# Kernel tuning notes

Hardware: AMD Instinct MI355X
Metric: run time of the kernel (lower is better)

Reference implementation:

```python
import jax, jax.numpy as jnp
import numpy as np

B, L, D = 2048, 96, 256  # groups, max group size, feature dim
COUNTS = np.tile(np.array([32, 64, 96, 64], dtype=np.int64), B // 4)  # ragged sizes, max=96
E = int(COUNTS.sum())  # 131072 edges


def setup_inputs() -> dict:
    key = jax.random.key(0)
    ks = jax.random.split(key, 12)
    s = 1.0 / np.sqrt(D)
    inp = {
        "x": jax.random.normal(ks[0], (E, D), jnp.float32),
        "timestamps_": jax.random.uniform(ks[1], (E,), jnp.float32),
    }
    names = ["w_ih_l0", "w_hh_l0", "b_ih_l0", "b_hh_l0",
             "w_ih_l1", "w_hh_l1", "b_ih_l1", "b_hh_l1"]
    shapes = [(3 * D, D), (3 * D, D), (3 * D,), (3 * D,),
              (3 * D, D), (3 * D, D), (3 * D,), (3 * D,)]
    for i, (n, sh) in enumerate(zip(names, shapes)):
        inp[n] = jax.random.uniform(ks[2 + i], sh, jnp.float32, -s, s)
    inp["index"] = jnp.asarray(np.repeat(np.arange(B), COUNTS), dtype=jnp.int32)
    return inp


def _gru_layer(seq, w_ih, w_hh, b_ih, b_hh):
    # seq: [B, L, F]; PyTorch gate order: r, z, n
    H = w_hh.shape[1]
    xp = jnp.einsum('blf,gf->blg', seq, w_ih) + b_ih  # precompute input GEMM, [B, L, 3H]

    def step(h, x_t):
        gh = h @ w_hh.T + b_hh  # [B, 3H]
        xr, xz, xn = jnp.split(x_t, 3, axis=-1)
        hr, hz, hn = jnp.split(gh, 3, axis=-1)
        r = jax.nn.sigmoid(xr + hr)
        z = jax.nn.sigmoid(xz + hz)
        n = jnp.tanh(xn + r * hn)
        h_new = (1 - z) * n + z * h
        return h_new, h_new

    h0 = jnp.zeros((seq.shape[0], H), seq.dtype)
    _, ys = jax.lax.scan(step, h0, jnp.swapaxes(xp, 0, 1))  # scan over time
    return jnp.swapaxes(ys, 0, 1)  # [B, L, H]


def reference(x, timestamps_, w_ih_l0, w_hh_l0, b_ih_l0, b_hh_l0,
              w_ih_l1, w_hh_l1, b_ih_l1, b_hh_l1, index):
    # prepend timestamp column: [E, D+1]
    feats = jnp.concatenate([timestamps_[:, None], x], axis=1)
    # to_dense_batch: sort by group, scatter into [B, L, D+1] (zero-padded)
    sort_ids = jnp.argsort(index)
    si = index[sort_ids]
    counts = jax.ops.segment_sum(jnp.ones((E,), jnp.int32), index, num_segments=B)
    offsets = jnp.cumsum(counts) - counts  # exclusive cumsum
    pos = jnp.arange(E, dtype=jnp.int32) - offsets[si]  # position within group
    dense = jnp.zeros((B, L, D + 1), feats.dtype).at[si, pos].set(feats[sort_ids])
    # sort each group by timestamp (column 0; padded zeros sort first), drop timestamp
    order = jnp.argsort(dense[:, :, 0], axis=1)
    seq = jnp.take_along_axis(dense, order[:, :, None], axis=1)[:, :, 1:]  # [B, L, D]
    # 2-layer GRU + mean pool over time
    h1 = _gru_layer(seq, w_ih_l0, w_hh_l0, b_ih_l0, b_hh_l0)
    h2 = _gru_layer(h1, w_ih_l1, w_hh_l1, b_ih_l1, b_hh_l1)
    return h2.mean(axis=1)  # [B, D] (squeeze is a no-op)
```

## Files before the change

kernel.cpp:

```cpp
#include <hip/hip_runtime.h>


typedef short bh8 __attribute__((ext_vector_type(8)));
typedef float f4  __attribute__((ext_vector_type(4)));

#define NB 2048
#define LT 96
#define DF 256
#define NG 768

#define LHA(col, row) (((((col) >> 5) * 64 + (((col) >> 3) & 3) * 16 + (row)) * 8) + ((col) & 7))

static __device__ __forceinline__ unsigned short f2b(float f) {
  union { float f; unsigned int u; } v; v.f = f;
  unsigned int r = v.u + 0x7fffu + ((v.u >> 16) & 1u);
  return (unsigned short)(r >> 16);
}
static __device__ __forceinline__ float b2f(unsigned short s) {
  union { unsigned int u; float f; } v; v.u = ((unsigned int)s) << 16; return v.f;
}
static __device__ __forceinline__ unsigned int pk2(float a, float b) {
  return (unsigned int)f2b(a) | ((unsigned int)f2b(b) << 16);
}
static __device__ __forceinline__ float sigm(float x) { return 1.0f / (1.0f + __expf(-x)); }
static __device__ __forceinline__ float tanh_(float x) { return 2.0f / (1.0f + __expf(-2.0f * x)) - 1.0f; }

__global__ void k_offsets(const int* __restrict__ idx, int E,
                          int* __restrict__ offs, int* __restrict__ cnt) {
  int b = blockIdx.x * blockDim.x + threadIdx.x;
  if (b >= NB) return;
  int lo = 0, hi = E;
  while (lo < hi) { int m = (lo + hi) >> 1; if (idx[m] < b) lo = m + 1; else hi = m; }
  int lb = lo;
  lo = lb; hi = E;
  while (lo < hi) { int m = (lo + hi) >> 1; if (idx[m] < b + 1) lo = m + 1; else hi = m; }
  offs[b] = lb;
  cnt[b] = lo - lb;
}

__global__ void k_rank(const float* __restrict__ ts, const int* __restrict__ offs,
                       const int* __restrict__ cnt, int* __restrict__ perm) {
  __shared__ float sts[96];
  int b = blockIdx.x, j = threadIdx.x;
  int o = offs[b];
  int c = cnt[b]; if (c > 96) c = 96;
  if (j < 96) perm[b * 96 + j] = -1;
  if (j < c) sts[j] = ts[o + j];
  __syncthreads();
  if (j < c) {
    float tj = sts[j];
    int rank = 0;
    for (int k = 0; k < c; ++k) {
      float tk = sts[k];
      rank += (tk < tj) || (tk == tj && k < j);
    }
    int slot = (tj > 0.0f ? (96 - c) : 0) + rank;
    perm[b * 96 + slot] = o + j;
  }
}

__global__ void k_packw(const float* __restrict__ w0, const float* __restrict__ w1,
                        const float* __restrict__ w2, const float* __restrict__ w3,
                        unsigned short* __restrict__ wfrag) {
  int t = blockIdx.x * blockDim.x + threadIdx.x;
  if (t >= 4 * 48 * 8 * 64) return;
  int m = t / 24576;
  int r = t % 24576;
  int nt = r / 512;
  int kt = (r / 64) & 7;
  int lane = r & 63;
  int n = nt * 16 + (lane & 15);
  int kb = kt * 32 + (lane >> 4) * 8;
  const float* W = (m == 0) ? w0 : (m == 1) ? w1 : (m == 2) ? w2 : w3;
  unsigned int o[4];
#pragma unroll
  for (int p = 0; p < 4; ++p)
    o[p] = pk2(W[n * 256 + kb + 2 * p], W[n * 256 + kb + 2 * p + 1]);
  uint4 v; v.x = o[0]; v.y = o[1]; v.z = o[2]; v.w = o[3];
  *(uint4*)&wfrag[(size_t)t * 8] = v;
}

template <int AMODE>
__launch_bounds__(256, 2)
__global__ void k_xgemm(const float* __restrict__ Ax, const unsigned short* __restrict__ Ab,
                        const int* __restrict__ perm, int t0, int slabsTotal, int jbN,
                        const unsigned short* __restrict__ wfrag, const float* __restrict__ bias,
                        unsigned short* __restrict__ Cout) {
  __shared__ float lsm[2][8960];

  const int tid = threadIdx.x;
  const int ntb = blockIdx.x % 6;
  const int jb  = blockIdx.x / 6;
  if (jb >= slabsTotal) return;
  const int w = tid >> 6, l = tid & 63, lm = l & 15, lq = l >> 4;

  const unsigned short* wfN = wfrag + (size_t)ntb * 32768;
  bh8 bf[2][8];
#pragma unroll
  for (int i = 0; i < 2; ++i)
#pragma unroll
    for (int kt = 0; kt < 8; ++kt)
      bf[i][kt] = *(const bh8*)&wfN[(((2 * w + i) * 8 + kt) * 64 + l) * 8];
  const float bias0 = bias[ntb * 128 + (2 * w + 0) * 16 + lm];
  const float bias1 = bias[ntb * 128 + (2 * w + 1) * 16 + lm];

  const int trow = tid >> 2, tp = tid & 3;
  const int msub = trow >> 4, rlm = trow & 15;

  f4 pf[16];
  uint4 pb[8];

  auto issue_loads = [&](int s) {
    int row = s * 64 + trow;
    if (AMODE == 0) {
      int tt = row >> 11, g = row & 2047;
      int src = perm[g * 96 + t0 + tt];
      if (src >= 0) {
        const float* p = Ax + (size_t)src * 256 + tp * 64;
#pragma unroll
        for (int i = 0; i < 16; ++i) pf[i] = *(const f4*)(p + 4 * i);
      } else {
#pragma unroll
        for (int i = 0; i < 16; ++i) pf[i] = (f4){0.f, 0.f, 0.f, 0.f};
      }
    } else {
      const unsigned short* p = Ab + (size_t)row * 256 + tp * 64;
#pragma unroll
      for (int i = 0; i < 8; ++i) pb[i] = *(const uint4*)(p + 8 * i);
    }
  };
  auto write_afrag = [&](int buf) {
    unsigned short* aN = (unsigned short*)lsm[buf];
#pragma unroll
    for (int kk = 0; kk < 2; ++kk)
#pragma unroll
      for (int rlq = 0; rlq < 4; ++rlq) {
        int kt = 2 * tp + kk;
        unsigned short* d = &aN[(((msub * 8 + kt) * 65) + rlq * 16 + rlm) * 8];
        if (AMODE == 0) {
          f4 f0 = pf[8 * kk + 2 * rlq], f1 = pf[8 * kk + 2 * rlq + 1];
          uint4 v;
          v.x = pk2(f0.x, f0.y); v.y = pk2(f0.z, f0.w);
          v.z = pk2(f1.x, f1.y); v.w = pk2(f1.z, f1.w);
          *(uint4*)d = v;
        } else {
          *(uint4*)d = pb[4 * kk + rlq];
        }
      }
  };

  issue_loads(jb);
  write_afrag(0);
  __syncthreads();

  int cur = 0;
  for (int s = jb; s < slabsTotal; s += jbN) {
    const int snext = s + jbN;
    const bool hasNext = snext < slabsTotal;
    if (hasNext) issue_loads(snext);

    const unsigned short* aC = (const unsigned short*)lsm[cur];
    f4 acc[4][2];
#pragma unroll
    for (int m = 0; m < 4; ++m)
#pragma unroll
      for (int n = 0; n < 2; ++n) acc[m][n] = (f4){0.f, 0.f, 0.f, 0.f};
#pragma unroll
    for (int kt = 0; kt < 8; ++kt) {
      bh8 a[4];
#pragma unroll
      for (int m = 0; m < 4; ++m) a[m] = *(const bh8*)&aC[(((m * 8 + kt) * 65) + l) * 8];
#pragma unroll
      for (int m = 0; m < 4; ++m) {
        acc[m][0] = __builtin_amdgcn_mfma_f32_16x16x32_bf16(a[m], bf[0][kt], acc[m][0], 0, 0, 0);
        acc[m][1] = __builtin_amdgcn_mfma_f32_16x16x32_bf16(a[m], bf[1][kt], acc[m][1], 0, 0, 0);
      }
    }

    float* sl = lsm[cur ^ 1];
#pragma unroll
    for (int m = 0; m < 4; ++m)
#pragma unroll
      for (int n = 0; n < 2; ++n) {
        int phys = 36 * w + 16 * n + lm;
        float bv = n ? bias1 : bias0;
#pragma unroll
        for (int r = 0; r < 4; ++r)
          sl[(m * 16 + lq * 4 + r) * 140 + phys] = acc[m][n][r] + bv;
      }
    __syncthreads();

    {
      const float* sp = &sl[trow * 140 + 36 * tp];
      unsigned short* cp = &Cout[((size_t)s * 64 + trow) * NG + ntb * 128 + tp * 32];
#pragma unroll
      for (int i = 0; i < 4; ++i) {
        f4 v0 = *(const f4*)(sp + 8 * i), v1 = *(const f4*)(sp + 8 * i + 4);
        uint4 o;
        o.x = pk2(v0.x, v0.y); o.y = pk2(v0.z, v0.w);
        o.z = pk2(v1.x, v1.y); o.w = pk2(v1.z, v1.w);
        *(uint4*)(cp + 8 * i) = o;
      }
    }
    __syncthreads();

    if (hasNext) {
      write_afrag(cur ^ 1);
      __syncthreads();
    }
    cur ^= 1;
  }
}

template <int LAYER>
__launch_bounds__(512, 2)
__global__ void k_recur(const unsigned short* __restrict__ wf, const float* __restrict__ bhh,
                        const unsigned short* __restrict__ xg, int Ta,
                        float* __restrict__ hstate, int first, int save,
                        unsigned short* __restrict__ h1out,
                        float* __restrict__ sumstate, float* __restrict__ outp, int last) {
  __shared__ __align__(16) unsigned short lBn[32768];
  __shared__ __align__(16) unsigned short lh[2][4096];
  __shared__ __align__(16) unsigned short lxg[2][6144];

  const int tid = threadIdx.x;
  const int w = tid >> 6, l = tid & 63, lm = l & 15, lq = l >> 4;
  const int g0 = blockIdx.x * 8;
  const int colA = w * 32 + lm;
  const int mycol = (lq < 2) ? colA : (colA + 16);
  const int rlow = (lq & 1) * 4;

  bh8 br0[8], br1[8], bz0[8], bz1[8], bn0[8];
#pragma unroll
  for (int kt = 0; kt < 8; ++kt) {
    br0[kt] = *(const bh8*)&wf[(((2 * w + 0) * 8 + kt) * 64 + l) * 8];
    br1[kt] = *(const bh8*)&wf[(((2 * w + 1) * 8 + kt) * 64 + l) * 8];
    bz0[kt] = *(const bh8*)&wf[(((16 + 2 * w) * 8 + kt) * 64 + l) * 8];
    bz1[kt] = *(const bh8*)&wf[(((17 + 2 * w) * 8 + kt) * 64 + l) * 8];
    bn0[kt] = *(const bh8*)&wf[(((32 + 2 * w) * 8 + kt) * 64 + l) * 8];
  }
  const float bhr = bhh[mycol];
  const float bhz = bhh[256 + mycol];
  const float bhn = bhh[512 + mycol];

  {
    for (int i = tid; i < 4096; i += 512) {
      int wp = i >> 9, kt = (i >> 6) & 7, lane = i & 63;
      ((uint4*)lBn)[i] = *(const uint4*)&wf[(((33 + 2 * wp) * 8 + kt) * 64 + lane) * 8];
    }
  }
  {
    uint4 z; z.x = 0u; z.y = 0u; z.z = 0u; z.w = 0u;
    for (int i = tid; i < 1024; i += 512) ((uint4*)lh)[i] = z;
  }
  __syncthreads();

  float hp[4], sm[4];
#pragma unroll
  for (int reg = 0; reg < 4; ++reg) {
    int row = rlow + reg;
    float a = first ? 0.f : hstate[(size_t)(g0 + row) * DF + mycol];
    hp[reg] = a;
    lh[0][LHA(mycol, row)] = f2b(a);
    lh[0][LHA(mycol, row + 8)] = f2b(a);
    if (LAYER == 1) {
      sm[reg] = (!first) ? sumstate[(size_t)(g0 + row) * DF + mycol] : 0.f;
    }
  }
  {
    const unsigned short* gp = xg + (size_t)g0 * NG;
    uint4 q0 = *(const uint4*)(gp + tid * 8);
    *(uint4*)&lxg[0][tid * 8] = q0;
    if (tid < 256) {
      uint4 q1 = *(const uint4*)(gp + 4096 + tid * 8);
      *(uint4*)&lxg[0][4096 + tid * 8] = q1;
    }
  }
  __syncthreads();

  int cur = 0;
  for (int tt = 0; tt < Ta; ++tt) {
    const int nxt = cur ^ 1;
    uint4 p0, p1;
    const bool hasN = (tt + 1 < Ta);
    if (hasN) {
      const unsigned short* gp = xg + ((size_t)(tt + 1) * NB + g0) * NG;
      p0 = *(const uint4*)(gp + tid * 8);
      if (tid < 256) p1 = *(const uint4*)(gp + 4096 + tid * 8);
    }
    if (LAYER == 0 && tt > 0 && tid < 256) {
      int row = tid >> 5, c0 = (tid & 31) * 8;
      uint4 hv = *(const uint4*)&lh[cur][(((c0 >> 5) * 64 + ((c0 >> 3) & 3) * 16 + row) * 8)];
      *(uint4*)&h1out[((size_t)(tt - 1) * NB + g0 + row) * DF + c0] = hv;
    }
    f4 ar0 = (f4){0.f,0.f,0.f,0.f}, ar1 = (f4){0.f,0.f,0.f,0.f};
    f4 az0 = (f4){0.f,0.f,0.f,0.f}, az1 = (f4){0.f,0.f,0.f,0.f};
    f4 an0 = (f4){0.f,0.f,0.f,0.f}, an1 = (f4){0.f,0.f,0.f,0.f};
    const unsigned short* hc = lh[cur];
#pragma unroll
    for (int kt = 0; kt < 8; ++kt) {
      bh8 a = *(const bh8*)&hc[(kt * 64 + l) * 8];
      ar0 = __builtin_amdgcn_mfma_f32_16x16x32_bf16(a, br0[kt], ar0, 0, 0, 0);
      ar1 = __builtin_amdgcn_mfma_f32_16x16x32_bf16(a, br1[kt], ar1, 0, 0, 0);
      az0 = __builtin_amdgcn_mfma_f32_16x16x32_bf16(a, bz0[kt], az0, 0, 0, 0);
      az1 = __builtin_amdgcn_mfma_f32_16x16x32_bf16(a, bz1[kt], az1, 0, 0, 0);
      an0 = __builtin_amdgcn_mfma_f32_16x16x32_bf16(a, bn0[kt], an0, 0, 0, 0);
      bh8 n1 = *(const bh8*)&lBn[((w * 8 + kt) * 64 + l) * 8];
      an1 = __builtin_amdgcn_mfma_f32_16x16x32_bf16(a, n1, an1, 0, 0, 0);
    }
    {
      f4 aR = (lq < 2) ? ar0 : ar1;
      f4 aZ = (lq < 2) ? az0 : az1;
      f4 aN = (lq < 2) ? an0 : an1;
      const unsigned short* xc = lxg[cur];
      unsigned short* hn = lh[nxt];
#pragma unroll
      for (int reg = 0; reg < 4; ++reg) {
        int row = rlow + reg;
        int base = row * NG + mycol;
        float xr = b2f(xc[base]);
        float xz = b2f(xc[base + 256]);
        float xn = b2f(xc[base + 512]);
        float r = sigm(xr + aR[reg] + bhr);
        float z = sigm(xz + aZ[reg] + bhz);
        float n = tanh_(xn + r * (aN[reg] + bhn));
        float h = (1.f - z) * n + z * hp[reg]; hp[reg] = h;
        unsigned short hb = f2b(h);
        hn[LHA(mycol, row)] = hb;
        hn[LHA(mycol, row + 8)] = hb;
        if (LAYER == 1) sm[reg] += h;
      }
    }
    if (hasN) {
      *(uint4*)&lxg[nxt][tid * 8] = p0;
      if (tid < 256) *(uint4*)&lxg[nxt][4096 + tid * 8] = p1;
    }
    __syncthreads();
    cur = nxt;
  }

  if (LAYER == 0 && tid < 256) {
    int row = tid >> 5, c0 = (tid & 31) * 8;
    uint4 hv = *(const uint4*)&lh[cur][(((c0 >> 5) * 64 + ((c0 >> 3) & 3) * 16 + row) * 8)];
    *(uint4*)&h1out[((size_t)(Ta - 1) * NB + g0 + row) * DF + c0] = hv;
  }
  if (save) {
#pragma unroll
    for (int reg = 0; reg < 4; ++reg) {
      int row = rlow + reg;
      hstate[(size_t)(g0 + row) * DF + mycol] = hp[reg];
    }
  }
  if (LAYER == 1) {
    if (last) {
#pragma unroll
      for (int reg = 0; reg < 4; ++reg) {
        int row = rlow + reg;
        outp[(size_t)(g0 + row) * DF + mycol] = sm[reg] * (1.0f / 96.0f);
      }
    } else {
#pragma unroll
      for (int reg = 0; reg < 4; ++reg) {
        int row = rlow + reg;
        sumstate[(size_t)(g0 + row) * DF + mycol] = sm[reg];
      }
    }
  }
}

extern "C" void kernel_launch(void* const* d_in, const int* in_sizes, int n_in,
                              void* d_out, int out_size, void* d_ws, size_t ws_size,
                              hipStream_t stream) {
  (void)n_in; (void)out_size;
  const float* x    = (const float*)d_in[0];
  const float* ts   = (const float*)d_in[1];
  const float* wih0 = (const float*)d_in[2];
  const float* whh0 = (const float*)d_in[3];
  const float* bih0 = (const float*)d_in[4];
  const float* bhh0 = (const float*)d_in[5];
  const float* wih1 = (const float*)d_in[6];
  const float* whh1 = (const float*)d_in[7];
  const float* bih1 = (const float*)d_in[8];
  const float* bhh1 = (const float*)d_in[9];
  const int*   idx  = (const int*)d_in[10];
  float* out = (float*)d_out;
  const int E = in_sizes[0] / DF;

  char* wsb = (char*)d_ws;
  size_t off = 0;
  auto carve = [&](size_t bytes) -> char* {
    off = (off + 255) & ~(size_t)255;
    char* p = wsb + off;
    off += bytes;
    return p;
  };
  int* offs = (int*)carve((size_t)NB * 4);
  int* cntp = (int*)carve((size_t)NB * 4);
  int* perm = (int*)carve((size_t)NB * LT * 4);
  unsigned short* wfrag = (unsigned short*)carve((size_t)4 * 196608 * 2);
  float* h0s  = (float*)carve((size_t)NB * DF * 4);
  float* h1s  = (float*)carve((size_t)NB * DF * 4);
  float* sums = (float*)carve((size_t)NB * DF * 4);
  size_t fixedBytes = off;

  const size_t perT = (size_t)NB * DF * 2 + 2 * (size_t)NB * NG * 2;
  int Tc = 1;
  if (ws_size > fixedBytes + 4096) {
    size_t t = (ws_size - fixedBytes - 4096) / perT;
    Tc = (int)(t > 96 ? 96 : (t < 1 ? 1 : t));
  }
  unsigned short* h1buf = (unsigned short*)carve((size_t)Tc * NB * DF * 2);
  unsigned short* xgA   = (unsigned short*)carve((size_t)Tc * NB * NG * 2);
  unsigned short* xgB   = (unsigned short*)carve((size_t)Tc * NB * NG * 2);

  k_offsets<<<8, 256, 0, stream>>>(idx, E, offs, cntp);
  k_rank<<<NB, 128, 0, stream>>>(ts, offs, cntp, perm);
  k_packw<<<384, 256, 0, stream>>>(wih0, whh0, wih1, whh1, wfrag);

  for (int t0 = 0; t0 < LT; t0 += Tc) {
    int Ta = (LT - t0 < Tc) ? (LT - t0) : Tc;
    int first = (t0 == 0);
    int save = (t0 + Ta < LT);
    int last = (t0 + Ta == LT);
    int slabs = Ta * 32;
    int jbN = slabs < 85 ? slabs : 85;
    k_xgemm<0><<<dim3(6 * jbN), 256, 0, stream>>>(
        x, (const unsigned short*)nullptr, perm, t0, slabs, jbN, wfrag, bih0, xgA);
    k_recur<0><<<256, 512, 0, stream>>>(
        wfrag + 1 * 196608, bhh0, xgA, Ta, h0s, first, save, h1buf,
        (float*)nullptr, (float*)nullptr, 0);
    k_xgemm<1><<<dim3(6 * jbN), 256, 0, stream>>>(
        (const float*)nullptr, h1buf, (const int*)nullptr, 0, slabs, jbN,
        wfrag + 2 * 196608, bih1, xgB);
    k_recur<1><<<256, 512, 0, stream>>>(
        wfrag + 3 * 196608, bhh1, xgB, Ta, h1s, first, save,
        (unsigned short*)nullptr, sums, out, last);
  }
}
```

Before: 1.099 ms.

## Prefetch recurrent input gates three steps ahead via direct global-to-LDS loads

The recurrent kernel now keeps the precomputed input-gate slices in a 4-deep LDS ring filled with global_load_lds, issued three timesteps ahead. Each step waits with hand-tuned per-wave vmcnt counts instead of staging through registers, which takes the global-load latency off the serial recurrence. The input-projection GEMM also walks its slabs in reverse order, probably so the first recurrent steps find their data still in cache. The hand-counted waits are fragile: they depend on how many outstanding vector memory ops each wave has, including the h1out stores in layer 0.

Measured after the change: 1.105 ms. About the same (+0.5%).

```diff
diff --git a/kernel.cpp b/kernel.cpp
--- a/kernel.cpp
+++ b/kernel.cpp
@@ -10,6 +10,27 @@
 #define NG 768
 
 #define LHA(col, row) (((((col) >> 5) * 64 + (((col) >> 3) & 3) * 16 + (row)) * 8) + ((col) & 7))
+
+#define LGKM0()  asm volatile("s_waitcnt lgkmcnt(0)" ::: "memory")
+#define SBAR()   __builtin_amdgcn_s_barrier()
+
+template <int N>
+static __device__ __forceinline__ void vmw() {
+  if constexpr (N == 0)      asm volatile("s_waitcnt vmcnt(0)" ::: "memory");
+  else if constexpr (N == 1) asm volatile("s_waitcnt vmcnt(1)" ::: "memory");
+  else if constexpr (N == 2) asm volatile("s_waitcnt vmcnt(2)" ::: "memory");
+  else if constexpr (N == 3) asm volatile("s_waitcnt vmcnt(3)" ::: "memory");
+  else if constexpr (N == 4) asm volatile("s_waitcnt vmcnt(4)" ::: "memory");
+  else if constexpr (N == 5) asm volatile("s_waitcnt vmcnt(5)" ::: "memory");
+  else if constexpr (N == 6) asm volatile("s_waitcnt vmcnt(6)" ::: "memory");
+  else                       asm volatile("s_waitcnt vmcnt(7)" ::: "memory");
+}
+
+static __device__ __forceinline__ void gl2lds16(const void* g, void* l) {
+  __builtin_amdgcn_global_load_lds(
+      (const __attribute__((address_space(1))) unsigned int*)g,
+      (__attribute__((address_space(3))) unsigned int*)l, 16, 0, 0);
+}
 
 static __device__ __forceinline__ unsigned short f2b(float f) {
   union { float f; unsigned int u; } v; v.f = f;
@@ -111,7 +132,7 @@
   uint4 pb[8];
 
   auto issue_loads = [&](int s) {
-    int row = s * 64 + trow;
+    int row = (slabsTotal - 1 - s) * 64 + trow;
     if (AMODE == 0) {
       int tt = row >> 11, g = row & 2047;
       int src = perm[g * 96 + t0 + tt];
@@ -192,7 +213,7 @@
 
     {
       const float* sp = &sl[trow * 140 + 36 * tp];
-      unsigned short* cp = &Cout[((size_t)s * 64 + trow) * NG + ntb * 128 + tp * 32];
+      unsigned short* cp = &Cout[((size_t)(slabsTotal - 1 - s) * 64 + trow) * NG + ntb * 128 + tp * 32];
 #pragma unroll
       for (int i = 0; i < 4; ++i) {
         f4 v0 = *(const f4*)(sp + 8 * i), v1 = *(const f4*)(sp + 8 * i + 4);
@@ -211,6 +232,64 @@
     cur ^= 1;
   }
 }
+
+#define RSTEP(TT, WLO, WHI, ISSUE, H1, WAIT)                                               \
+  {                                                                                        \
+    if (LAYER == 0 && (H1) && tid < 256) {                                                 \
+      int rw_ = tid >> 5, c0_ = (tid & 31) * 8;                                            \
+      uint4 hv_ = *(const uint4*)&lh[(TT) & 1][(((c0_ >> 5) * 64 + ((c0_ >> 3) & 3) * 16 + rw_) * 8)]; \
+      *(uint4*)&h1out[((size_t)((TT) - 1) * NB + g0 + rw_) * DF + c0_] = hv_;              \
+    }                                                                                      \
+    if (ISSUE) {                                                                           \
+      const unsigned short* gp_ = xg + ((size_t)((TT) + 3) * NB + g0) * NG;                \
+      unsigned short* lb_ = lxg[((TT) + 3) & 3];                                           \
+      gl2lds16(gp_ + (size_t)tid * 8, lb_ + 512 * w);                                      \
+      if (tid < 256) gl2lds16(gp_ + 4096 + (size_t)tid * 8, lb_ + 4096 + 512 * w);         \
+    }                                                                                      \
+    f4 ar0 = (f4){0.f,0.f,0.f,0.f}, ar1 = (f4){0.f,0.f,0.f,0.f};                           \
+    f4 az0 = (f4){0.f,0.f,0.f,0.f}, az1 = (f4){0.f,0.f,0.f,0.f};                           \
+    f4 an0 = (f4){0.f,0.f,0.f,0.f}, an1 = (f4){0.f,0.f,0.f,0.f};                           \
+    {                                                                                      \
+      const unsigned short* hc_ = lh[(TT) & 1];                                            \
+      _Pragma("unroll")                                                                    \
+      for (int kt = 0; kt < 8; ++kt) {                                                     \
+        bh8 a_ = *(const bh8*)&hc_[(kt * 64 + l) * 8];                                     \
+        ar0 = __builtin_amdgcn_mfma_f32_16x16x32_bf16(a_, br0[kt], ar0, 0, 0, 0);          \
+        ar1 = __builtin_amdgcn_mfma_f32_16x16x32_bf16(a_, br1[kt], ar1, 0, 0, 0);          \
+        az0 = __builtin_amdgcn_mfma_f32_16x16x32_bf16(a_, bz0[kt], az0, 0, 0, 0);          \
+        az1 = __builtin_amdgcn_mfma_f32_16x16x32_bf16(a_, bz1[kt], az1, 0, 0, 0);          \
+        an0 = __builtin_amdgcn_mfma_f32_16x16x32_bf16(a_, bn0[kt], an0, 0, 0, 0);          \
+        bh8 n1_ = *(const bh8*)&lBn[((w * 8 + kt) * 64 + l) * 8];                          \
+        an1 = __builtin_amdgcn_mfma_f32_16x16x32_bf16(a_, n1_, an1, 0, 0, 0);              \
+      }                                                                                    \
+    }                                                                                      \
+    {                                                                                      \
+      f4 aR = (lq < 2) ? ar0 : ar1;                                                        \
+      f4 aZ = (lq < 2) ? az0 : az1;                                                        \
+      f4 aN = (lq < 2) ? an0 : an1;                                                        \
+      const unsigned short* xc_ = lxg[(TT) & 3];                                           \
+      unsigned short* hn_ = lh[((TT) & 1) ^ 1];                                            \
+      _Pragma("unroll")                                                                    \
+      for (int reg = 0; reg < 4; ++reg) {                                                  \
+        int row_ = rlow + reg;                                                             \
+        int base_ = row_ * NG + mycol;                                                     \
+        float xr_ = b2f(xc_[base_]);                                                       \
+        float xz_ = b2f(xc_[base_ + 256]);                                                 \
+        float xn_ = b2f(xc_[base_ + 512]);                                                 \
+        float r_ = sigm(xr_ + aR[reg] + bhr);                                              \
+        float z_ = sigm(xz_ + aZ[reg] + bhz);                                              \
+        float n_ = tanh_(xn_ + r_ * (aN[reg] + bhn));                                      \
+        float h_ = (1.f - z_) * n_ + z_ * hp[reg]; hp[reg] = h_;                           \
+        unsigned short hb_ = f2b(h_);                                                      \
+        hn_[LHA(mycol, row_)] = hb_;                                                       \
+        hn_[LHA(mycol, row_ + 8)] = hb_;                                                   \
+        if (LAYER == 1) sm[reg] += h_;                                                     \
+      }                                                                                    \
+    }                                                                                      \
+    LGKM0();                                                                               \
+    if (WAIT) { if (w < 4) { vmw<(WLO)>(); } else { vmw<(WHI)>(); } }                      \
+    SBAR();                                                                                \
+  }
 
 template <int LAYER>
 __launch_bounds__(512, 2)
@@ -221,7 +300,7 @@
                         float* __restrict__ sumstate, float* __restrict__ outp, int last) {
   __shared__ __align__(16) unsigned short lBn[32768];
   __shared__ __align__(16) unsigned short lh[2][4096];
-  __shared__ __align__(16) unsigned short lxg[2][6144];
+  __shared__ __align__(16) unsigned short lxg[4][6144];
 
   const int tid = threadIdx.x;
   const int w = tid >> 6, l = tid & 63, lm = l & 15, lq = l >> 4;
@@ -263,85 +342,50 @@
     hp[reg] = a;
     lh[0][LHA(mycol, row)] = f2b(a);
     lh[0][LHA(mycol, row + 8)] = f2b(a);
-    if (LAYER == 1) {
-      sm[reg] = (!first) ? sumstate[(size_t)(g0 + row) * DF + mycol] : 0.f;
-    }
-  }
-  {
-    const unsigned short* gp = xg + (size_t)g0 * NG;
-    uint4 q0 = *(const uint4*)(gp + tid * 8);
-    *(uint4*)&lxg[0][tid * 8] = q0;
-    if (tid < 256) {
-      uint4 q1 = *(const uint4*)(gp + 4096 + tid * 8);
-      *(uint4*)&lxg[0][4096 + tid * 8] = q1;
-    }
+    if (LAYER == 1) sm[reg] = (!first) ? sumstate[(size_t)(g0 + row) * DF + mycol] : 0.f;
   }
   __syncthreads();
 
-  int cur = 0;
-  for (int tt = 0; tt < Ta; ++tt) {
-    const int nxt = cur ^ 1;
-    uint4 p0, p1;
-    const bool hasN = (tt + 1 < Ta);
-    if (hasN) {
-      const unsigned short* gp = xg + ((size_t)(tt + 1) * NB + g0) * NG;
-      p0 = *(const uint4*)(gp + tid * 8);
-      if (tid < 256) p1 = *(const uint4*)(gp + 4096 + tid * 8);
-    }
-    if (LAYER == 0 && tt > 0 && tid < 256) {
-      int row = tid >> 5, c0 = (tid & 31) * 8;
-      uint4 hv = *(const uint4*)&lh[cur][(((c0 >> 5) * 64 + ((c0 >> 3) & 3) * 16 + row) * 8)];
-      *(uint4*)&h1out[((size_t)(tt - 1) * NB + g0 + row) * DF + c0] = hv;
-    }
-    f4 ar0 = (f4){0.f,0.f,0.f,0.f}, ar1 = (f4){0.f,0.f,0.f,0.f};
-    f4 az0 = (f4){0.f,0.f,0.f,0.f}, az1 = (f4){0.f,0.f,0.f,0.f};
-    f4 an0 = (f4){0.f,0.f,0.f,0.f}, an1 = (f4){0.f,0.f,0.f,0.f};
-    const unsigned short* hc = lh[cur];
-#pragma unroll
-    for (int kt = 0; kt < 8; ++kt) {
-      bh8 a = *(const bh8*)&hc[(kt * 64 + l) * 8];
-      ar0 = __builtin_amdgcn_mfma_f32_16x16x32_bf16(a, br0[kt], ar0, 0, 0, 0);
-      ar1 = __builtin_amdgcn_mfma_f32_16x16x32_bf16(a, br1[kt], ar1, 0, 0, 0);
-      az0 = __builtin_amdgcn_mfma_f32_16x16x32_bf16(a, bz0[kt], az0, 0, 0, 0);
-      az1 = __builtin_amdgcn_mfma_f32_16x16x32_bf16(a, bz1[kt], az1, 0, 0, 0);
-      an0 = __builtin_amdgcn_mfma_f32_16x16x32_bf16(a, bn0[kt], an0, 0, 0, 0);
-      bh8 n1 = *(const bh8*)&lBn[((w * 8 + kt) * 64 + l) * 8];
-      an1 = __builtin_amdgcn_mfma_f32_16x16x32_bf16(a, n1, an1, 0, 0, 0);
-    }
-    {
-      f4 aR = (lq < 2) ? ar0 : ar1;
-      f4 aZ = (lq < 2) ? az0 : az1;
-      f4 aN = (lq < 2) ? an0 : an1;
-      const unsigned short* xc = lxg[cur];
-      unsigned short* hn = lh[nxt];
-#pragma unroll
-      for (int reg = 0; reg < 4; ++reg) {
-        int row = rlow + reg;
-        int base = row * NG + mycol;
-        float xr = b2f(xc[base]);
-        float xz = b2f(xc[base + 256]);
-        float xn = b2f(xc[base + 512]);
-        float r = sigm(xr + aR[reg] + bhr);
-        float z = sigm(xz + aZ[reg] + bhz);
-        float n = tanh_(xn + r * (aN[reg] + bhn));
-        float h = (1.f - z) * n + z * hp[reg]; hp[reg] = h;
-        unsigned short hb = f2b(h);
-        hn[LHA(mycol, row)] = hb;
-        hn[LHA(mycol, row + 8)] = hb;
-        if (LAYER == 1) sm[reg] += h;
-      }
-    }
-    if (hasN) {
-      *(uint4*)&lxg[nxt][tid * 8] = p0;
-      if (tid < 256) *(uint4*)&lxg[nxt][4096 + tid * 8] = p1;
-    }
-    __syncthreads();
-    cur = nxt;
-  }
-
+  if (Ta >= 6) {
+#pragma unroll
+    for (int k = 0; k < 3; ++k) {
+      const unsigned short* gp = xg + ((size_t)k * NB + g0) * NG;
+      unsigned short* lb = lxg[k];
+      gl2lds16(gp + (size_t)tid * 8, lb + 512 * w);
+      if (tid < 256) gl2lds16(gp + 4096 + (size_t)tid * 8, lb + 4096 + 512 * w);
+    }
+    LGKM0();
+    if (w < 4) { vmw<4>(); } else { vmw<2>(); }
+    SBAR();
+
+    RSTEP(0, 4, 2, true, false, true);
+    RSTEP(1, (LAYER == 0 ? 5 : 4), 2, true, true, true);
+    for (int tt = 2; tt <= Ta - 4; ++tt) {
+      RSTEP(tt, (LAYER == 0 ? 6 : 4), 2, true, true, true);
+    }
+    RSTEP(Ta - 3, (LAYER == 0 ? 4 : 2), 1, false, true, true);
+    RSTEP(Ta - 2, (LAYER == 0 ? 2 : 0), 0, false, true, true);
+    RSTEP(Ta - 1, 0, 0, false, true, false);
+  } else {
+#pragma unroll
+    for (int k = 0; k < 3; ++k) {
+      if (k < Ta) {
+        const unsigned short* gp = xg + ((size_t)k * NB + g0) * NG;
+        unsigned short* lb = lxg[k];
+        gl2lds16(gp + (size_t)tid * 8, lb + 512 * w);
+        if (tid < 256) gl2lds16(gp + 4096 + (size_t)tid * 8, lb + 4096 + 512 * w);
+      }
+    }
+    LGKM0(); vmw<0>(); SBAR();
+    for (int tt = 0; tt < Ta; ++tt) {
+      RSTEP(tt, 0, 0, (tt + 3 < Ta), (tt >= 1), (tt + 1 < Ta));
+    }
+  }
+
+  const unsigned short* lhf = lh[Ta & 1];
   if (LAYER == 0 && tid < 256) {
     int row = tid >> 5, c0 = (tid & 31) * 8;
-    uint4 hv = *(const uint4*)&lh[cur][(((c0 >> 5) * 64 + ((c0 >> 3) & 3) * 16 + row) * 8)];
+    uint4 hv = *(const uint4*)&lhf[(((c0 >> 5) * 64 + ((c0 >> 3) & 3) * 16 + row) * 8)];
     *(uint4*)&h1out[((size_t)(Ta - 1) * NB + g0 + row) * DF + c0] = hv;
   }
   if (save) {
```
